# Optimization experiments

Hardware: AMD Instinct MI355X
Metric: run time of the kernel (lower is better)

The kernel has to match this reference:

```python
import jax, jax.numpy as jnp
import numpy as np

B, S, C = 8, 2048, 512

def setup_inputs() -> dict:
    key = jax.random.key(0)
    ks = jax.random.split(key, 7)
    s = 1.0 / np.sqrt(C)
    return {
        "x": jax.random.normal(ks[0], (B, S, C), dtype=jnp.float32),
        "Wq": jax.random.uniform(ks[1], (C, C), jnp.float32, -s, s),
        "bq": jax.random.uniform(ks[2], (C,), jnp.float32, -s, s),
        "Wk": jax.random.uniform(ks[3], (C, C), jnp.float32, -s, s),
        "bk": jax.random.uniform(ks[4], (C,), jnp.float32, -s, s),
        "Wv": jax.random.uniform(ks[5], (C, C), jnp.float32, -s, s),
        "bv": jax.random.uniform(ks[6], (C,), jnp.float32, -s, s),
    }

def reference(x, Wq, bq, Wk, bk, Wv, bv):
    # Linear projections (torch Linear: x @ W.T + b)
    q = jnp.einsum('bsc,dc->bsd', x, Wq) + bq
    k = jnp.einsum('bsc,dc->bsd', x, Wk) + bk
    v = jnp.einsum('bsc,dc->bsd', x, Wv) + bv
    # NOTE: original code computes dk but never scales by 1/sqrt(dk)
    scores = jnp.einsum('bqd,bkd->bqk', q, k)          # [B,S,S]
    attn = jax.nn.softmax(scores, axis=-1)
    out = jnp.einsum('bqk,bkd->bqd', attn, v)
    return out + x
```

## Files before the change

### kernel.cpp

```cpp
#include <hip/hip_runtime.h>
#include <hip/hip_bf16.h>


typedef __bf16 bf16_t;
typedef bf16_t bf16x8 __attribute__((ext_vector_type(8)));
typedef float floatx4 __attribute__((ext_vector_type(4)));

#define MFMA16(a, b, c) __builtin_amdgcn_mfma_f32_16x16x32_bf16((a), (b), (c), 0, 0, 0)
#define FLASH_LDS 140800

__device__ __forceinline__ void gload16(const void* g, void* l) {
    __builtin_amdgcn_global_load_lds((const __attribute__((address_space(1))) void*)g,
                                     (__attribute__((address_space(3))) void*)l, 16, 0, 0);
}

__device__ __forceinline__ float wave16_sum(float v) {
    v += __shfl_xor(v, 1);
    v += __shfl_xor(v, 2);
    v += __shfl_xor(v, 4);
    v += __shfl_xor(v, 8);
    return v;
}

__global__ void convert_in(const float* __restrict__ X,
                           const float* __restrict__ Wq, const float* __restrict__ Wk,
                           const float* __restrict__ Wv, const float* __restrict__ bq,
                           const float* __restrict__ bk, const float* __restrict__ bv,
                           bf16_t* __restrict__ Xb, bf16_t* __restrict__ Wb,
                           float* __restrict__ biasc) {
    int bid = blockIdx.x, tid = threadIdx.x;
    if (bid < 4096) {
        size_t e0 = ((size_t)bid * 256 + tid) * 8;
        float4 f0 = *(const float4*)(X + e0);
        float4 f1 = *(const float4*)(X + e0 + 4);
        bf16x8 o;
        o[0] = (bf16_t)f0.x; o[1] = (bf16_t)f0.y; o[2] = (bf16_t)f0.z; o[3] = (bf16_t)f0.w;
        o[4] = (bf16_t)f1.x; o[5] = (bf16_t)f1.y; o[6] = (bf16_t)f1.z; o[7] = (bf16_t)f1.w;
        *(bf16x8*)(Xb + e0) = o;
    } else {
        int idx = (bid - 4096) * 256 + tid;
        int e0 = idx * 4;
        int row = e0 >> 9, c = e0 & 511;
        const float* src;
        if (row < 512)       src = Wq + row * 512;
        else if (row < 1024) src = Wk + (row - 512) * 512;
        else                 src = Wv + (row - 1024) * 512;
        float4 v = *(const float4*)(src + c);
        Wb[e0 + 0] = (bf16_t)v.x;
        Wb[e0 + 1] = (bf16_t)v.y;
        Wb[e0 + 2] = (bf16_t)v.z;
        Wb[e0 + 3] = (bf16_t)v.w;
        if (idx < 1536) {
            float b;
            if (idx < 512)       b = bq[idx];
            else if (idx < 1024) b = bk[idx - 512];
            else                 b = bv[idx - 1024];
            biasc[idx] = b;
        }
    }
}

__global__ __launch_bounds__(256, 2)
void qkv_gemm(const bf16_t* __restrict__ Xb, const bf16_t* __restrict__ Wb,
              const float* __restrict__ biasc, bf16_t* __restrict__ Q,
              bf16_t* __restrict__ K, bf16_t* __restrict__ Vt) {
    __shared__ int4 smem4[2560];
    char* As = (char*)smem4;
    char* Bs = (char*)smem4 + 16384;
    char* Vtile = (char*)smem4;

    const int tid = threadIdx.x;
    const int l = tid & 63, w = tid >> 6;
    const int lane16 = l & 15, lq = l >> 4;
    const int klo = lane16 & 7;
    const int m0 = (blockIdx.x & 127) << 7;
    const int n0 = (blockIdx.x >> 7) << 7;
    const int wm = (w >> 1) << 6, wn = (w & 1) << 6;
    const int srow = l >> 3;
    const int sc8 = (l & 7) ^ srow;

    floatx4 acc[4][4];
#pragma unroll
    for (int a = 0; a < 4; ++a)
#pragma unroll
        for (int bb = 0; bb < 4; ++bb) acc[a][bb] = (floatx4){0.f, 0.f, 0.f, 0.f};

    for (int it = 0; it < 8; ++it) {
        __syncthreads();
#pragma unroll
        for (int j = 0; j < 4; ++j) {
            int seg = j * 4 + w;
            int row = seg * 8 + srow;
            gload16(Xb + (size_t)(m0 + row) * 512 + it * 64 + sc8 * 8, As + seg * 1024);
            gload16(Wb + (size_t)(n0 + row) * 512 + it * 64 + sc8 * 8, Bs + seg * 1024);
        }
        __syncthreads();
#pragma unroll
        for (int kst = 0; kst < 2; ++kst) {
            bf16x8 afr[4], bfr[4];
#pragma unroll
            for (int mt = 0; mt < 4; ++mt)
                afr[mt] = *(const bf16x8*)(As + (wm + mt * 16 + lane16) * 128 +
                                           ((kst * 4 + lq) ^ klo) * 16);
#pragma unroll
            for (int nt = 0; nt < 4; ++nt)
                bfr[nt] = *(const bf16x8*)(Bs + (wn + nt * 16 + lane16) * 128 +
                                           ((kst * 4 + lq) ^ klo) * 16);
#pragma unroll
            for (int mt = 0; mt < 4; ++mt)
#pragma unroll
                for (int nt = 0; nt < 4; ++nt)
                    acc[mt][nt] = MFMA16(afr[mt], bfr[nt], acc[mt][nt]);
        }
    }

    float bias_v[4];
#pragma unroll
    for (int nt = 0; nt < 4; ++nt) bias_v[nt] = biasc[n0 + wn + nt * 16 + lane16];

    if (n0 < 1024) {
        bf16_t* Dst = (n0 < 512) ? Q : K;
        const int coff = (n0 < 512 ? n0 : n0 - 512) + wn;
#pragma unroll
        for (int mt = 0; mt < 4; ++mt)
#pragma unroll
            for (int nt = 0; nt < 4; ++nt)
#pragma unroll
                for (int i = 0; i < 4; ++i) {
                    int rowM = m0 + wm + mt * 16 + lq * 4 + i;
                    Dst[(size_t)rowM * 512 + coff + nt * 16 + lane16] =
                        (bf16_t)(acc[mt][nt][i] + bias_v[nt]);
                }
    } else {
        __syncthreads();
#pragma unroll
        for (int mt = 0; mt < 4; ++mt)
#pragma unroll
            for (int nt = 0; nt < 4; ++nt)
#pragma unroll
                for (int i = 0; i < 4; ++i) {
                    int dl = wn + nt * 16 + lane16;
                    int sl = wm + mt * 16 + lq * 4 + i;
                    *(bf16_t*)(Vtile + dl * 264 + sl * 2) =
                        (bf16_t)(acc[mt][nt][i] + bias_v[nt]);
                }
        __syncthreads();
        const int bb = m0 >> 11, s0 = m0 & 2047, dbase = n0 - 1024;
#pragma unroll
        for (int j = 0; j < 8; ++j) {
            int slot = j * 256 + tid;
            int dd = slot >> 4, c = slot & 15;
            *(int4*)(Vt + (size_t)(bb * 512 + dbase + dd) * 2048 + s0 + c * 8) =
                *(const int4*)(Vtile + dd * 264 + c * 16);
        }
    }
}

__global__ __launch_bounds__(512, 2)
void flash_attn_v3(const bf16_t* __restrict__ Q, const bf16_t* __restrict__ K,
                   const bf16_t* __restrict__ Vt, const float* __restrict__ X,
                   float* __restrict__ Out) {
    extern __shared__ char smem[];
    char* Ks = smem;
    char* Vs = smem + 65536;
    char* Ps = smem + 131072;
    float* lpart = (float*)(smem + 140288);

    const int tid = threadIdx.x;
    const int l = tid & 63, w = tid >> 6;
    const int lane16 = l & 15, lq = l >> 4;
    const int qg = w >> 1, h = w & 1;
    const int dbase = w << 6;
    const int b = blockIdx.x & 7;
    const int q0 = (blockIdx.x >> 3) << 6;

    const bf16_t* Kbase = K + (size_t)b * 2048 * 512;
    const bf16_t* Vbase = Vt + (size_t)b * 512 * 2048;

#pragma unroll
    for (int j = 0; j < 8; ++j) {
        int seg = j * 8 + w;
        int c = (l & ~7) | ((l & 7) ^ (seg & 7));
        gload16(Kbase + (size_t)seg * 512 + c * 8, Ks + seg * 1024);
    }

    bf16x8 qf[16];
    const bf16_t* Qrow = Q + (size_t)(b * 2048 + q0 + qg * 16 + lane16) * 512 + lq * 8;
#pragma unroll
    for (int kst = 0; kst < 16; ++kst) qf[kst] = *(const bf16x8*)(Qrow + kst * 32);

    floatx4 o[16];
#pragma unroll
    for (int t = 0; t < 16; ++t) o[t] = (floatx4){0.f, 0.f, 0.f, 0.f};
    float lsum[4] = {0.f, 0.f, 0.f, 0.f};
    const float L2E = 1.4426950408889634f;

    __syncthreads();

    for (int kt = 0; kt < 32; ++kt) {
        {
            const bf16_t* Vsrc = Vbase + kt * 64;
#pragma unroll
            for (int j = 0; j < 8; ++j) {
                int seg = j * 8 + w;
                int d = seg * 8 + (l >> 3);
                int c = (l & 7) ^ (l >> 3);
                gload16(Vsrc + (size_t)d * 2048 + c * 8, Vs + seg * 1024);
            }
        }
        floatx4 scA[2], scB[2];
#pragma unroll
        for (int g = 0; g < 2; ++g) {
            scA[g] = (floatx4){0.f, 0.f, 0.f, 0.f};
            scB[g] = (floatx4){0.f, 0.f, 0.f, 0.f};
        }
#pragma unroll
        for (int kst = 0; kst < 16; kst += 2) {
#pragma unroll
            for (int g = 0; g < 2; ++g) {
                int key = h * 32 + g * 16 + lane16;
                int i0 = kst * 4 + lq;
                int i1 = i0 + 4;
                int p0 = (i0 & ~7) | ((i0 & 7) ^ (key & 7));
                int p1 = (i1 & ~7) | ((i1 & 7) ^ (key & 7));
                bf16x8 kb0 = *(const bf16x8*)(Ks + key * 1024 + p0 * 16);
                bf16x8 kb1 = *(const bf16x8*)(Ks + key * 1024 + p1 * 16);
                scA[g] = MFMA16(qf[kst], kb0, scA[g]);
                scB[g] = MFMA16(qf[kst + 1], kb1, scB[g]);
            }
        }
#pragma unroll
        for (int g = 0; g < 2; ++g) {
            int keyc = h * 32 + g * 16 + lane16;
#pragma unroll
            for (int i = 0; i < 4; ++i) {
                float p = __builtin_exp2f((scA[g][i] + scB[g][i]) * L2E);
                lsum[i] += p;
                *(bf16_t*)(Ps + (qg * 16 + lq * 4 + i) * 144 + keyc * 2) = (bf16_t)p;
            }
        }
        __syncthreads();

        if (kt < 31) {
            const bf16_t* Ksrc = Kbase + (size_t)(kt + 1) * 64 * 512;
#pragma unroll
            for (int j = 0; j < 8; ++j) {
                int seg = j * 8 + w;
                int c = (l & ~7) | ((l & 7) ^ (seg & 7));
                gload16(Ksrc + (size_t)seg * 512 + c * 8, Ks + seg * 1024);
            }
        }
#pragma unroll
        for (int kk = 0; kk < 2; ++kk) {
            bf16x8 pa[4];
#pragma unroll
            for (int qgi = 0; qgi < 4; ++qgi)
                pa[qgi] = *(const bf16x8*)(Ps + (qgi * 16 + lane16) * 144 + kk * 64 + lq * 16);
#pragma unroll
            for (int dg = 0; dg < 4; ++dg) {
                int d = dbase + dg * 16 + lane16;
                int pos = (kk * 4 + lq) ^ (d & 7);
                bf16x8 vb = *(const bf16x8*)(Vs + d * 128 + pos * 16);
#pragma unroll
                for (int qgi = 0; qgi < 4; ++qgi)
                    o[qgi * 4 + dg] = MFMA16(pa[qgi], vb, o[qgi * 4 + dg]);
            }
        }
        __syncthreads();
    }

#pragma unroll
    for (int i = 0; i < 4; ++i) {
        float s = wave16_sum(lsum[i]);
        if (lane16 == 0) lpart[(qg * 16 + lq * 4 + i) * 2 + h] = s;
    }
    __syncthreads();

#pragma unroll
    for (int qgi = 0; qgi < 4; ++qgi) {
        float rinv[4];
#pragma unroll
        for (int i = 0; i < 4; ++i) {
            int row = qgi * 16 + lq * 4 + i;
            rinv[i] = 1.0f / (lpart[row * 2] + lpart[row * 2 + 1]);
        }
#pragma unroll
        for (int dg = 0; dg < 4; ++dg) {
            int d = dbase + dg * 16 + lane16;
#pragma unroll
            for (int i = 0; i < 4; ++i) {
                int row = q0 + qgi * 16 + lq * 4 + i;
                size_t g = (size_t)(b * 2048 + row) * 512 + d;
                Out[g] = o[qgi * 4 + dg][i] * rinv[i] + X[g];
            }
        }
    }
}

extern "C" void kernel_launch(void* const* d_in, const int* in_sizes, int n_in,
                              void* d_out, int out_size, void* d_ws, size_t ws_size,
                              hipStream_t stream) {
    const float* x  = (const float*)d_in[0];
    const float* Wq = (const float*)d_in[1];
    const float* bq = (const float*)d_in[2];
    const float* Wk = (const float*)d_in[3];
    const float* bk = (const float*)d_in[4];
    const float* Wv = (const float*)d_in[5];
    const float* bv = (const float*)d_in[6];
    float* out = (float*)d_out;
    char* ws = (char*)d_ws;

    bf16_t* Wb    = (bf16_t*)(ws);
    float*  biasc = (float*)(ws + 1572864);
    bf16_t* Xb    = (bf16_t*)(ws + 1579008);
    bf16_t* Qb    = (bf16_t*)(ws + 18356224);
    bf16_t* Kb    = (bf16_t*)(ws + 35133440);
    bf16_t* Vt    = (bf16_t*)(ws + 51910656);

    convert_in<<<4864, 256, 0, stream>>>(x, Wq, Wk, Wv, bq, bk, bv, Xb, Wb, biasc);
    qkv_gemm<<<1536, 256, 0, stream>>>(Xb, Wb, biasc, Qb, Kb, Vt);

    hipFuncSetAttribute(reinterpret_cast<const void*>(flash_attn_v3),
                        hipFuncAttributeMaxDynamicSharedMemorySize, FLASH_LDS);
    flash_attn_v3<<<256, 512, FLASH_LDS, stream>>>(Qb, Kb, Vt, x, out);
}
```

Baseline: 210.1 us.

## Stage Q/K GEMM output through LDS and rebalance QK^T wave tiling

The QKV GEMM epilogue for Q and K now writes the tile into LDS and stores it with coalesced 16-byte rows, replacing scattered 2-byte global stores. The V transpose tile pitch changes to 272 bytes to match. In the attention kernel, each wave now computes scores for 32 query rows against 16 keys instead of 16 rows against 32 keys. This reuses each K fragment read from LDS across two MFMAs, cutting LDS traffic. The costs are twice the Q fragment registers per wave and a four-way partial row-sum reduction, which needs slightly more LDS.

```diff
diff --git a/kernel.cpp b/kernel.cpp
--- a/kernel.cpp
+++ b/kernel.cpp
@@ -7,7 +7,7 @@
 typedef float floatx4 __attribute__((ext_vector_type(4)));
 
 #define MFMA16(a, b, c) __builtin_amdgcn_mfma_f32_16x16x32_bf16((a), (b), (c), 0, 0, 0)
-#define FLASH_LDS 140800
+#define FLASH_LDS 141312
 
 __device__ __forceinline__ void gload16(const void* g, void* l) {
     __builtin_amdgcn_global_load_lds((const __attribute__((address_space(1))) void*)g,
@@ -67,7 +67,7 @@
     __shared__ int4 smem4[2560];
     char* As = (char*)smem4;
     char* Bs = (char*)smem4 + 16384;
-    char* Vtile = (char*)smem4;
+    char* Ctile = (char*)smem4;
 
     const int tid = threadIdx.x;
     const int l = tid & 63, w = tid >> 6;
@@ -118,21 +118,31 @@
 #pragma unroll
     for (int nt = 0; nt < 4; ++nt) bias_v[nt] = biasc[n0 + wn + nt * 16 + lane16];
 
+    __syncthreads();
+
     if (n0 < 1024) {
-        bf16_t* Dst = (n0 < 512) ? Q : K;
-        const int coff = (n0 < 512 ? n0 : n0 - 512) + wn;
 #pragma unroll
         for (int mt = 0; mt < 4; ++mt)
 #pragma unroll
             for (int nt = 0; nt < 4; ++nt)
 #pragma unroll
                 for (int i = 0; i < 4; ++i) {
-                    int rowM = m0 + wm + mt * 16 + lq * 4 + i;
-                    Dst[(size_t)rowM * 512 + coff + nt * 16 + lane16] =
+                    int rl = wm + mt * 16 + lq * 4 + i;
+                    int cl = wn + nt * 16 + lane16;
+                    *(bf16_t*)(Ctile + rl * 272 + cl * 2) =
                         (bf16_t)(acc[mt][nt][i] + bias_v[nt]);
                 }
+        __syncthreads();
+        bf16_t* Dst = (n0 < 512) ? Q : K;
+        const int coff = (n0 < 512) ? n0 : (n0 - 512);
+#pragma unroll
+        for (int j = 0; j < 8; ++j) {
+            int slot = j * 256 + tid;
+            int row = slot >> 4, c = slot & 15;
+            *(int4*)(Dst + (size_t)(m0 + row) * 512 + coff + c * 8) =
+                *(const int4*)(Ctile + row * 272 + c * 16);
+        }
     } else {
-        __syncthreads();
 #pragma unroll
         for (int mt = 0; mt < 4; ++mt)
 #pragma unroll
@@ -141,7 +151,7 @@
                 for (int i = 0; i < 4; ++i) {
                     int dl = wn + nt * 16 + lane16;
                     int sl = wm + mt * 16 + lq * 4 + i;
-                    *(bf16_t*)(Vtile + dl * 264 + sl * 2) =
+                    *(bf16_t*)(Ctile + dl * 272 + sl * 2) =
                         (bf16_t)(acc[mt][nt][i] + bias_v[nt]);
                 }
         __syncthreads();
@@ -151,13 +161,13 @@
             int slot = j * 256 + tid;
             int dd = slot >> 4, c = slot & 15;
             *(int4*)(Vt + (size_t)(bb * 512 + dbase + dd) * 2048 + s0 + c * 8) =
-                *(const int4*)(Vtile + dd * 264 + c * 16);
+                *(const int4*)(Ctile + dd * 272 + c * 16);
         }
     }
 }
 
 __global__ __launch_bounds__(512, 2)
-void flash_attn_v3(const bf16_t* __restrict__ Q, const bf16_t* __restrict__ K,
+void flash_attn_v4(const bf16_t* __restrict__ Q, const bf16_t* __restrict__ K,
                    const bf16_t* __restrict__ Vt, const float* __restrict__ X,
                    float* __restrict__ Out) {
     extern __shared__ char smem[];
@@ -169,7 +179,7 @@
     const int tid = threadIdx.x;
     const int l = tid & 63, w = tid >> 6;
     const int lane16 = l & 15, lq = l >> 4;
-    const int qg = w >> 1, h = w & 1;
+    const int qh = w >> 2, kq = w & 3;
     const int dbase = w << 6;
     const int b = blockIdx.x & 7;
     const int q0 = (blockIdx.x >> 3) << 6;
@@ -184,16 +194,24 @@
         gload16(Kbase + (size_t)seg * 512 + c * 8, Ks + seg * 1024);
     }
 
-    bf16x8 qf[16];
-    const bf16_t* Qrow = Q + (size_t)(b * 2048 + q0 + qg * 16 + lane16) * 512 + lq * 8;
-#pragma unroll
-    for (int kst = 0; kst < 16; ++kst) qf[kst] = *(const bf16x8*)(Qrow + kst * 32);
+    bf16x8 qf0[16], qf1[16];
+    const bf16_t* Qr0 = Q + (size_t)(b * 2048 + q0 + qh * 32 + lane16) * 512 + lq * 8;
+#pragma unroll
+    for (int kst = 0; kst < 16; ++kst) {
+        qf0[kst] = *(const bf16x8*)(Qr0 + kst * 32);
+        qf1[kst] = *(const bf16x8*)(Qr0 + 16 * 512 + kst * 32);
+    }
 
     floatx4 o[16];
 #pragma unroll
     for (int t = 0; t < 16; ++t) o[t] = (floatx4){0.f, 0.f, 0.f, 0.f};
-    float lsum[4] = {0.f, 0.f, 0.f, 0.f};
+    float ls0[4] = {0.f, 0.f, 0.f, 0.f};
+    float ls1[4] = {0.f, 0.f, 0.f, 0.f};
     const float L2E = 1.4426950408889634f;
+
+    const int key = kq * 16 + lane16;
+    const char* kptr = Ks + key * 1024;
+    const int k7 = key & 7;
 
     __syncthreads();
 
@@ -208,36 +226,32 @@
                 gload16(Vsrc + (size_t)d * 2048 + c * 8, Vs + seg * 1024);
             }
         }
-        floatx4 scA[2], scB[2];
-#pragma unroll
-        for (int g = 0; g < 2; ++g) {
-            scA[g] = (floatx4){0.f, 0.f, 0.f, 0.f};
-            scB[g] = (floatx4){0.f, 0.f, 0.f, 0.f};
-        }
+        floatx4 s0a = (floatx4){0.f, 0.f, 0.f, 0.f};
+        floatx4 s0b = (floatx4){0.f, 0.f, 0.f, 0.f};
+        floatx4 s1a = (floatx4){0.f, 0.f, 0.f, 0.f};
+        floatx4 s1b = (floatx4){0.f, 0.f, 0.f, 0.f};
 #pragma unroll
         for (int kst = 0; kst < 16; kst += 2) {
-#pragma unroll
-            for (int g = 0; g < 2; ++g) {
-                int key = h * 32 + g * 16 + lane16;
-                int i0 = kst * 4 + lq;
-                int i1 = i0 + 4;
-                int p0 = (i0 & ~7) | ((i0 & 7) ^ (key & 7));
-                int p1 = (i1 & ~7) | ((i1 & 7) ^ (key & 7));
-                bf16x8 kb0 = *(const bf16x8*)(Ks + key * 1024 + p0 * 16);
-                bf16x8 kb1 = *(const bf16x8*)(Ks + key * 1024 + p1 * 16);
-                scA[g] = MFMA16(qf[kst], kb0, scA[g]);
-                scB[g] = MFMA16(qf[kst + 1], kb1, scB[g]);
-            }
-        }
-#pragma unroll
-        for (int g = 0; g < 2; ++g) {
-            int keyc = h * 32 + g * 16 + lane16;
-#pragma unroll
-            for (int i = 0; i < 4; ++i) {
-                float p = __builtin_exp2f((scA[g][i] + scB[g][i]) * L2E);
-                lsum[i] += p;
-                *(bf16_t*)(Ps + (qg * 16 + lq * 4 + i) * 144 + keyc * 2) = (bf16_t)p;
-            }
+            int i0 = kst * 4 + lq;
+            int i1 = i0 + 4;
+            int p0 = (i0 & ~7) | ((i0 & 7) ^ k7);
+            int p1 = (i1 & ~7) | ((i1 & 7) ^ k7);
+            bf16x8 kb0 = *(const bf16x8*)(kptr + p0 * 16);
+            bf16x8 kb1 = *(const bf16x8*)(kptr + p1 * 16);
+            s0a = MFMA16(qf0[kst], kb0, s0a);
+            s0b = MFMA16(qf0[kst + 1], kb1, s0b);
+            s1a = MFMA16(qf1[kst], kb0, s1a);
+            s1b = MFMA16(qf1[kst + 1], kb1, s1b);
+        }
+#pragma unroll
+        for (int i = 0; i < 4; ++i) {
+            float p0 = __builtin_exp2f((s0a[i] + s0b[i]) * L2E);
+            float p1 = __builtin_exp2f((s1a[i] + s1b[i]) * L2E);
+            ls0[i] += p0;
+            ls1[i] += p1;
+            int row0 = qh * 32 + lq * 4 + i;
+            *(bf16_t*)(Ps + row0 * 144 + key * 2) = (bf16_t)p0;
+            *(bf16_t*)(Ps + (row0 + 16) * 144 + key * 2) = (bf16_t)p1;
         }
         __syncthreads();
 
@@ -271,8 +285,12 @@
 
 #pragma unroll
     for (int i = 0; i < 4; ++i) {
-        float s = wave16_sum(lsum[i]);
-        if (lane16 == 0) lpart[(qg * 16 + lq * 4 + i) * 2 + h] = s;
+        float s0 = wave16_sum(ls0[i]);
+        float s1 = wave16_sum(ls1[i]);
+        if (lane16 == 0) {
+            lpart[(qh * 32 + lq * 4 + i) * 4 + kq] = s0;
+            lpart[(qh * 32 + 16 + lq * 4 + i) * 4 + kq] = s1;
+        }
     }
     __syncthreads();
 
@@ -282,7 +300,8 @@
 #pragma unroll
         for (int i = 0; i < 4; ++i) {
             int row = qgi * 16 + lq * 4 + i;
-            rinv[i] = 1.0f / (lpart[row * 2] + lpart[row * 2 + 1]);
+            float4 l4 = *(float4*)&lpart[row * 4];
+            rinv[i] = 1.0f / (l4.x + l4.y + l4.z + l4.w);
         }
 #pragma unroll
         for (int dg = 0; dg < 4; ++dg) {
@@ -320,7 +339,7 @@
     convert_in<<<4864, 256, 0, stream>>>(x, Wq, Wk, Wv, bq, bk, bv, Xb, Wb, biasc);
     qkv_gemm<<<1536, 256, 0, stream>>>(Xb, Wb, biasc, Qb, Kb, Vt);
 
-    hipFuncSetAttribute(reinterpret_cast<const void*>(flash_attn_v3),
+    hipFuncSetAttribute(reinterpret_cast<const void*>(flash_attn_v4),
                         hipFuncAttributeMaxDynamicSharedMemorySize, FLASH_LDS);
-    flash_attn_v3<<<256, 512, FLASH_LDS, stream>>>(Qb, Kb, Vt, x, out);
-}
+    flash_attn_v4<<<256, 512, FLASH_LDS, stream>>>(Qb, Kb, Vt, x, out);
+}
```

Result: slower. 254.4 us (+21.1%).

## Double-buffer K and P in LDS, load V directly to registers, one barrier per tile

Applied to the files above, without the earlier changes.

The flash attention kernel now keeps two LDS buffers for K and for P, so the next K tile is prefetched at the start of each iteration while the current one is consumed. V is no longer staged through LDS. Each wave reads its V fragments straight from global memory into registers before the barrier. The per-iteration barrier count drops from two to one. This trades more LDS (about 150KB) and more registers, plus uncoalesced direct global V reads, for better overlap and less synchronisation.

```diff
diff --git a/kernel.cpp b/kernel.cpp
--- a/kernel.cpp
+++ b/kernel.cpp
@@ -7,7 +7,7 @@
 typedef float floatx4 __attribute__((ext_vector_type(4)));
 
 #define MFMA16(a, b, c) __builtin_amdgcn_mfma_f32_16x16x32_bf16((a), (b), (c), 0, 0, 0)
-#define FLASH_LDS 140800
+#define FLASH_LDS 150016
 
 __device__ __forceinline__ void gload16(const void* g, void* l) {
     __builtin_amdgcn_global_load_lds((const __attribute__((address_space(1))) void*)g,
@@ -157,14 +157,13 @@
 }
 
 __global__ __launch_bounds__(512, 2)
-void flash_attn_v3(const bf16_t* __restrict__ Q, const bf16_t* __restrict__ K,
+void flash_attn_v5(const bf16_t* __restrict__ Q, const bf16_t* __restrict__ K,
                    const bf16_t* __restrict__ Vt, const float* __restrict__ X,
                    float* __restrict__ Out) {
     extern __shared__ char smem[];
-    char* Ks = smem;
-    char* Vs = smem + 65536;
-    char* Ps = smem + 131072;
-    float* lpart = (float*)(smem + 140288);
+    char* Ks0 = smem;
+    char* Ps0 = smem + 131072;
+    float* lpart = (float*)(smem + 149504);
 
     const int tid = threadIdx.x;
     const int l = tid & 63, w = tid >> 6;
@@ -181,7 +180,7 @@
     for (int j = 0; j < 8; ++j) {
         int seg = j * 8 + w;
         int c = (l & ~7) | ((l & 7) ^ (seg & 7));
-        gload16(Kbase + (size_t)seg * 512 + c * 8, Ks + seg * 1024);
+        gload16(Kbase + (size_t)seg * 512 + c * 8, Ks0 + seg * 1024);
     }
 
     bf16x8 qf[16];
@@ -198,16 +197,21 @@
     __syncthreads();
 
     for (int kt = 0; kt < 32; ++kt) {
-        {
-            const bf16_t* Vsrc = Vbase + kt * 64;
+        const int cur = kt & 1;
+        char* Ks = Ks0 + cur * 65536;
+        char* Ps = Ps0 + cur * 9216;
+
+        if (kt < 31) {
+            char* Kn = Ks0 + (1 - cur) * 65536;
+            const bf16_t* Ksrc = Kbase + (size_t)(kt + 1) * 64 * 512;
 #pragma unroll
             for (int j = 0; j < 8; ++j) {
                 int seg = j * 8 + w;
-                int d = seg * 8 + (l >> 3);
-                int c = (l & 7) ^ (l >> 3);
-                gload16(Vsrc + (size_t)d * 2048 + c * 8, Vs + seg * 1024);
-            }
-        }
+                int c = (l & ~7) | ((l & 7) ^ (seg & 7));
+                gload16(Ksrc + (size_t)seg * 512 + c * 8, Kn + seg * 1024);
+            }
+        }
+
         floatx4 scA[2], scB[2];
 #pragma unroll
         for (int g = 0; g < 2; ++g) {
@@ -229,6 +233,7 @@
                 scB[g] = MFMA16(qf[kst + 1], kb1, scB[g]);
             }
         }
+
 #pragma unroll
         for (int g = 0; g < 2; ++g) {
             int keyc = h * 32 + g * 16 + lane16;
@@ -239,17 +244,19 @@
                 *(bf16_t*)(Ps + (qg * 16 + lq * 4 + i) * 144 + keyc * 2) = (bf16_t)p;
             }
         }
-        __syncthreads();
-
-        if (kt < 31) {
-            const bf16_t* Ksrc = Kbase + (size_t)(kt + 1) * 64 * 512;
-#pragma unroll
-            for (int j = 0; j < 8; ++j) {
-                int seg = j * 8 + w;
-                int c = (l & ~7) | ((l & 7) ^ (seg & 7));
-                gload16(Ksrc + (size_t)seg * 512 + c * 8, Ks + seg * 1024);
-            }
-        }
+
+        bf16x8 vb[2][4];
+#pragma unroll
+        for (int kk = 0; kk < 2; ++kk)
+#pragma unroll
+            for (int dg = 0; dg < 4; ++dg) {
+                int d = dbase + dg * 16 + lane16;
+                vb[kk][dg] = *(const bf16x8*)(Vbase + (size_t)d * 2048 +
+                                              kt * 64 + kk * 32 + lq * 8);
+            }
+
+        __syncthreads();
+
 #pragma unroll
         for (int kk = 0; kk < 2; ++kk) {
             bf16x8 pa[4];
@@ -257,16 +264,11 @@
             for (int qgi = 0; qgi < 4; ++qgi)
                 pa[qgi] = *(const bf16x8*)(Ps + (qgi * 16 + lane16) * 144 + kk * 64 + lq * 16);
 #pragma unroll
-            for (int dg = 0; dg < 4; ++dg) {
-                int d = dbase + dg * 16 + lane16;
-                int pos = (kk * 4 + lq) ^ (d & 7);
-                bf16x8 vb = *(const bf16x8*)(Vs + d * 128 + pos * 16);
+            for (int dg = 0; dg < 4; ++dg)
 #pragma unroll
                 for (int qgi = 0; qgi < 4; ++qgi)
-                    o[qgi * 4 + dg] = MFMA16(pa[qgi], vb, o[qgi * 4 + dg]);
-            }
-        }
-        __syncthreads();
+                    o[qgi * 4 + dg] = MFMA16(pa[qgi], vb[kk][dg], o[qgi * 4 + dg]);
+        }
     }
 
 #pragma unroll
@@ -320,7 +322,7 @@
     convert_in<<<4864, 256, 0, stream>>>(x, Wq, Wk, Wv, bq, bk, bv, Xb, Wb, biasc);
     qkv_gemm<<<1536, 256, 0, stream>>>(Xb, Wb, biasc, Qb, Kb, Vt);
 
-    hipFuncSetAttribute(reinterpret_cast<const void*>(flash_attn_v3),
+    hipFuncSetAttribute(reinterpret_cast<const void*>(flash_attn_v5),
                         hipFuncAttributeMaxDynamicSharedMemorySize, FLASH_LDS);
-    flash_attn_v3<<<256, 512, FLASH_LDS, stream>>>(Qb, Kb, Vt, x, out);
-}
+    flash_attn_v5<<<256, 512, FLASH_LDS, stream>>>(Qb, Kb, Vt, x, out);
+}
```

After: 235.3 us. 1.12x slower.
